# Kernel tuning notes

Hardware: AMD Instinct MI355X
Metric: run time of the kernel (lower is better)

The kernel has to match this reference:

```python
import jax, jax.numpy as jnp
import numpy as np
from jax import lax

B, P, ENC = 64, 196, 2048
E, H, A, V = 512, 512, 512, 10000
L = 21  # caption length -> T = 20 decode steps


def setup_inputs() -> dict:
    key = jax.random.key(0)
    ks = jax.random.split(key, 20)
    s = 0.02
    inp = {
        "features": jax.random.normal(ks[0], (B, P, ENC), jnp.float32),
        "captions": jax.random.randint(ks[1], (B, L), 0, V),
        # attention
        "W_enc_att": jax.random.normal(ks[2], (ENC, A), jnp.float32) * s,
        "b_enc_att": jnp.zeros((A,), jnp.float32),
        "W_dec_att": jax.random.normal(ks[3], (H, A), jnp.float32) * s,
        "b_dec_att": jnp.zeros((A,), jnp.float32),
        "W_full": jax.random.normal(ks[4], (A, 1), jnp.float32) * s,
        "b_full": jnp.zeros((1,), jnp.float32),
        # embedding (uniform(-0.1, 0.1) as in init_weights)
        "emb": jax.random.uniform(ks[5], (V, E), jnp.float32, -0.1, 0.1),
        # LSTMCell: input = embed + encoder_dim, gate order i,f,g,o
        "W_ih": jax.random.normal(ks[6], (E + ENC, 4 * H), jnp.float32) * s,
        "W_hh": jax.random.normal(ks[7], (H, 4 * H), jnp.float32) * s,
        "b_ih": jnp.zeros((4 * H,), jnp.float32),
        "b_hh": jnp.zeros((4 * H,), jnp.float32),
        # init state projections
        "W_init_h": jax.random.normal(ks[8], (ENC, H), jnp.float32) * s,
        "b_init_h": jnp.zeros((H,), jnp.float32),
        "W_init_c": jax.random.normal(ks[9], (ENC, H), jnp.float32) * s,
        "b_init_c": jnp.zeros((H,), jnp.float32),
        # gating
        "W_fbeta": jax.random.normal(ks[10], (H, ENC), jnp.float32) * s,
        "b_fbeta": jnp.zeros((ENC,), jnp.float32),
        # output fc (uniform(-0.1,0.1), bias 0)
        "W_fc": jax.random.uniform(ks[11], (H, V), jnp.float32, -0.1, 0.1),
        "b_fc": jnp.zeros((V,), jnp.float32),
    }
    return inp


def reference(features, captions, W_enc_att, b_enc_att, W_dec_att, b_dec_att,
              W_full, b_full, emb, W_ih, W_hh, b_ih, b_hh,
              W_init_h, b_init_h, W_init_c, b_init_c,
              W_fbeta, b_fbeta, W_fc, b_fc):
    # init hidden state from mean-pooled encoder features
    mean_enc = features.mean(axis=1)                       # [B, ENC]
    h0 = mean_enc @ W_init_h + b_init_h                    # [B, H]
    c0 = mean_enc @ W_init_c + b_init_c

    # encoder-side attention projection is time-invariant: precompute
    att1 = features @ W_enc_att + b_enc_att                # [B, P, A]

    T = captions.shape[1] - 1                              # decode_lengths = L-1 (equal lengths)
    embs = emb[captions[:, :T]]                            # [B, T, E]
    embs_t = jnp.swapaxes(embs, 0, 1)                      # [T, B, E]

    def step(carry, e_t):
        h, c = carry
        att2 = h @ W_dec_att + b_dec_att                   # [B, A]
        scores = (jax.nn.relu(att1 + att2[:, None, :]) @ W_full)[..., 0] + b_full  # [B, P]
        alpha = jax.nn.softmax(scores, axis=1)
        awe = jnp.einsum('bp,bpe->be', alpha, features)    # [B, ENC]
        gate = jax.nn.sigmoid(h @ W_fbeta + b_fbeta)
        awe = gate * awe
        x = jnp.concatenate([e_t, awe], axis=1)            # [B, E+ENC]
        gates = x @ W_ih + h @ W_hh + b_ih + b_hh          # [B, 4H]
        i, f, g, o = jnp.split(gates, 4, axis=1)
        c_new = jax.nn.sigmoid(f) * c + jax.nn.sigmoid(i) * jnp.tanh(g)
        h_new = jax.nn.sigmoid(o) * jnp.tanh(c_new)
        preds = h_new @ W_fc + b_fc                        # dropout in eval mode = identity
        return (h_new, c_new), preds

    _, preds = lax.scan(step, (h0, c0), embs_t)            # [T, B, V]
    return jnp.swapaxes(preds, 0, 1)                       # [B, T, V]
```

## Files before the change

kernel.cpp:

```cpp
#include <hip/hip_runtime.h>
#include <hip/hip_bf16.h>


#define TB 256

typedef __bf16 bf16x8 __attribute__((ext_vector_type(8)));
typedef float f32x4 __attribute__((ext_vector_type(4)));
typedef unsigned short u16x8 __attribute__((ext_vector_type(8)));
typedef unsigned short u16x4 __attribute__((ext_vector_type(4)));
typedef unsigned short ushort_t;

__device__ __forceinline__ ushort_t f2bf(float x) {
    unsigned u = __builtin_bit_cast(unsigned, x);
    u += 0x7fffu + ((u >> 16) & 1u);
    return (ushort_t)(u >> 16);
}
__device__ __forceinline__ float bf2f(ushort_t b) {
    return __builtin_bit_cast(float, (unsigned)b << 16);
}
__device__ __forceinline__ void store_pack(
    ushort_t* __restrict__ Ph, ushort_t* __restrict__ Pl,
    int KC, int m, int k, float v)
{
    const size_t flat = ((((size_t)(m >> 4) * KC + (k >> 5)) * 64)
                         + ((k & 31) >> 3) * 16 + (m & 15)) * 8 + (k & 7);
    const ushort_t h = f2bf(v);
    Ph[flat] = h;
    Pl[flat] = f2bf(v - bf2f(h));
}

struct PackJobs {
    const float* W[7];
    ushort_t* Bh[7];
    ushort_t* Bl[7];
    int Nsrc[7], ntCount[7], KC[7], ntBase[7];
    int cum[8];
};

__global__ __launch_bounds__(TB) void pack_all(PackJobs J)
{
    const int blk = blockIdx.x;
    int j = 0;
    #pragma unroll
    for (int i = 1; i < 7; ++i) if (blk >= J.cum[i]) j = i;
    const int g = (blk - J.cum[j]) * TB + threadIdx.x;
    const int KC = J.KC[j];
    const int lane = g & 63;
    const int kc = (g >> 6) % KC;
    const int nt = g / (64 * KC);
    if (nt >= J.ntCount[j]) return;
    const int Nsrc = J.Nsrc[j];
    const float* W = J.W[j];
    const int n = nt * 16 + (lane & 15);
    const int kb = kc * 32 + (lane >> 4) * 8;
    u16x8 hv, lv;
    #pragma unroll
    for (int e = 0; e < 8; ++e) {
        const float x = (n < Nsrc) ? W[(size_t)(kb + e) * Nsrc + n] : 0.f;
        const ushort_t h = f2bf(x);
        hv[e] = h;
        lv[e] = f2bf(x - bf2f(h));
    }
    const size_t flat = (((size_t)(J.ntBase[j] + nt) * KC + kc) * 64 + lane) * 8;
    *(u16x8*)&J.Bh[j][flat] = hv;
    *(u16x8*)&J.Bl[j][flat] = lv;
}

__global__ __launch_bounds__(TB) void feat2bf(
    const float* __restrict__ f, ushort_t* __restrict__ fbf)
{
    const size_t i8 = ((size_t)blockIdx.x * TB + threadIdx.x) * 8;
    const float4 a = *(const float4*)&f[i8];
    const float4 b = *(const float4*)&f[i8 + 4];
    u16x8 v;
    v[0] = f2bf(a.x); v[1] = f2bf(a.y); v[2] = f2bf(a.z); v[3] = f2bf(a.w);
    v[4] = f2bf(b.x); v[5] = f2bf(b.y); v[6] = f2bf(b.z); v[7] = f2bf(b.w);
    *(u16x8*)&fbf[i8] = v;
}

template<int MT, int NT, int WR, int WC>
__device__ __forceinline__ void mfma_tile(
    const ushort_t* lds, int wr, int wc, int lane,
    f32x4 acc[MT / WR][NT / WC])
{
    constexpr int MFR = MT / WR, NFR = NT / WC;
    bf16x8 ah[MFR], al[MFR];
    #pragma unroll
    for (int i = 0; i < MFR; ++i) {
        ah[i] = __builtin_bit_cast(bf16x8, *(const u16x8*)&lds[(wr * MFR + i) * 512 + lane * 8]);
        al[i] = __builtin_bit_cast(bf16x8, *(const u16x8*)&lds[(MT + wr * MFR + i) * 512 + lane * 8]);
    }
    #pragma unroll
    for (int j = 0; j < NFR; ++j) {
        const bf16x8 bh = __builtin_bit_cast(bf16x8, *(const u16x8*)&lds[(2 * MT + wc * NFR + j) * 512 + lane * 8]);
        const bf16x8 bl = __builtin_bit_cast(bf16x8, *(const u16x8*)&lds[(2 * MT + NT + wc * NFR + j) * 512 + lane * 8]);
        #pragma unroll
        for (int i = 0; i < MFR; ++i) {
            acc[i][j] = __builtin_amdgcn_mfma_f32_16x16x32_bf16(ah[i], bh, acc[i][j], 0, 0, 0);
            acc[i][j] = __builtin_amdgcn_mfma_f32_16x16x32_bf16(ah[i], bl, acc[i][j], 0, 0, 0);
            acc[i][j] = __builtin_amdgcn_mfma_f32_16x16x32_bf16(al[i], bh, acc[i][j], 0, 0, 0);
        }
    }
}

template<int MT, int NT, int WR, int WC>
__global__ __launch_bounds__(TB) void gemm_mfma(
    const ushort_t* __restrict__ Ah, const ushort_t* __restrict__ Al,
    const ushort_t* __restrict__ Bh, const ushort_t* __restrict__ Bl,
    int KC, int kcPer,
    const float* __restrict__ bias,
    float* __restrict__ C, int ldc, int Ncols, size_t cPartStride)
{
    constexpr int MFR = MT / WR, NFR = NT / WC, CH = 2 * (MT + NT);
    __shared__ __align__(16) ushort_t lds[CH * 512];
    const int tid = threadIdx.x, wid = tid >> 6, lane = tid & 63;
    const int wr = wid / WC, wc = wid % WC;

    const int tot = gridDim.x * gridDim.y;
    const int lin = blockIdx.x + gridDim.x * blockIdx.y;
    const int q = tot >> 3, r = tot & 7;
    const int xcd = lin & 7, jj = lin >> 3;
    const int base = (xcd < r) ? xcd * (q + 1) : r * (q + 1) + (xcd - r) * q;
    const int lin2 = base + jj;
    const int nb = lin2 / gridDim.y;
    const int mb = lin2 % gridDim.y;

    const int kc0 = blockIdx.z * kcPer;

    f32x4 acc[MFR][NFR];
    #pragma unroll
    for (int i = 0; i < MFR; ++i)
        #pragma unroll
        for (int j = 0; j < NFR; ++j)
            acc[i][j] = f32x4{0.f, 0.f, 0.f, 0.f};

    for (int kc = kc0; kc < kc0 + kcPer; ++kc) {
        __syncthreads();
        #pragma unroll
        for (int cc = 0; cc < CH / 4; ++cc) {
            const int c = cc * 4 + wid;
            const ushort_t* src;
            if (c < MT)                src = Ah + ((size_t)(mb * MT + c) * KC + kc) * 512;
            else if (c < 2 * MT)       src = Al + ((size_t)(mb * MT + c - MT) * KC + kc) * 512;
            else if (c < 2 * MT + NT)  src = Bh + ((size_t)(nb * NT + c - 2 * MT) * KC + kc) * 512;
            else                       src = Bl + ((size_t)(nb * NT + c - 2 * MT - NT) * KC + kc) * 512;
            *(u16x8*)&lds[c * 512 + lane * 8] = *(const u16x8*)(src + lane * 8);
        }
        __syncthreads();
        mfma_tile<MT, NT, WR, WC>(lds, wr, wc, lane, acc);
    }

    C += (size_t)blockIdx.z * cPartStride;
    #pragma unroll
    for (int i = 0; i < MFR; ++i)
        #pragma unroll
        for (int j = 0; j < NFR; ++j) {
            const int col = nb * NT * 16 + (wc * NFR + j) * 16 + (lane & 15);
            if (col < Ncols) {
                const float bv = bias ? bias[col] : 0.f;
                const int rbase = mb * MT * 16 + (wr * MFR + i) * 16 + ((lane >> 4) << 2);
                #pragma unroll
                for (int r2 = 0; r2 < 4; ++r2)
                    C[(size_t)(rbase + r2) * ldc + col] = acc[i][j][r2] + bv;
            }
        }
}

__global__ __launch_bounds__(TB) void gemm_att1(
    const ushort_t* __restrict__ fbf,
    const ushort_t* __restrict__ Bh, const ushort_t* __restrict__ Bl,
    const float* __restrict__ bias, ushort_t* __restrict__ att1bf)
{
    __shared__ __align__(16) ushort_t lds[2 * 16 * 512];
    const int tid = threadIdx.x, wid = tid >> 6, lane = tid & 63;
    const int wr = wid >> 1, wc = wid & 1;

    const int lin = blockIdx.x + (blockIdx.y << 3);
    const int lin2 = (lin & 7) * 98 + (lin >> 3);
    const int nb = lin2 & 7, mb = lin2 >> 3;

    f32x4 acc[4][2];
    #pragma unroll
    for (int i = 0; i < 4; ++i)
        #pragma unroll
        for (int j = 0; j < 2; ++j)
            acc[i][j] = f32x4{0.f, 0.f, 0.f, 0.f};

    const int akg = tid & 3;
    const size_t abase = (size_t)(mb * 128) * 2048;

    u16x8 rA[4], rB[4];

    auto issueTo = [&](int kc, u16x8* r) {
        #pragma unroll
        for (int cc = 0; cc < 2; ++cc) {
            const int c = cc * 4 + wid;
            const ushort_t* src = (c < 4)
                ? Bh + ((size_t)(nb * 4 + c) * 64 + kc) * 512
                : Bl + ((size_t)(nb * 4 + (c - 4)) * 64 + kc) * 512;
            r[cc] = *(const u16x8*)(src + lane * 8);
        }
        #pragma unroll
        for (int p = 0; p < 2; ++p) {
            const int row = (p * 256 + tid) >> 2;
            r[2 + p] = *(const u16x8*)&fbf[abase + (size_t)row * 2048 + (size_t)kc * 32 + akg * 8];
        }
    };
    auto commitFrom = [&](const u16x8* r, ushort_t* buf) {
        #pragma unroll
        for (int cc = 0; cc < 2; ++cc) {
            const int c = cc * 4 + wid;
            *(u16x8*)&buf[(8 + c) * 512 + lane * 8] = r[cc];
        }
        #pragma unroll
        for (int p = 0; p < 2; ++p) {
            const int row = (p * 256 + tid) >> 2;
            *(u16x8*)&buf[(row >> 4) * 512 + (akg * 16 + (row & 15)) * 8] = r[2 + p];
        }
    };
    auto compute = [&](const ushort_t* buf) {
        bf16x8 ah[4];
        #pragma unroll
        for (int i = 0; i < 4; ++i)
            ah[i] = __builtin_bit_cast(bf16x8, *(const u16x8*)&buf[(wr * 4 + i) * 512 + lane * 8]);
        #pragma unroll
        for (int j = 0; j < 2; ++j) {
            const bf16x8 bh = __builtin_bit_cast(bf16x8, *(const u16x8*)&buf[(8 + wc * 2 + j) * 512 + lane * 8]);
            const bf16x8 bl = __builtin_bit_cast(bf16x8, *(const u16x8*)&buf[(12 + wc * 2 + j) * 512 + lane * 8]);
            #pragma unroll
            for (int i = 0; i < 4; ++i) {
                acc[i][j] = __builtin_amdgcn_mfma_f32_16x16x32_bf16(ah[i], bh, acc[i][j], 0, 0, 0);
                acc[i][j] = __builtin_amdgcn_mfma_f32_16x16x32_bf16(ah[i], bl, acc[i][j], 0, 0, 0);
            }
        }
    };

    issueTo(0, rA);
    commitFrom(rA, lds);
    issueTo(1, rB);
    __syncthreads();

    for (int kc = 0; kc < 64; kc += 2) {
        if (kc + 2 < 64) issueTo(kc + 2, rA);
        compute(lds);
        commitFrom(rB, lds + 16 * 512);
        __syncthreads();
        if (kc + 3 < 64) issueTo(kc + 3, rB);
        compute(lds + 16 * 512);
        if (kc + 2 < 64) commitFrom(rA, lds);
        __syncthreads();
    }

    #pragma unroll
    for (int i = 0; i < 4; ++i)
        #pragma unroll
        for (int j = 0; j < 2; ++j) {
            const int col = nb * 64 + (wc * 2 + j) * 16 + (lane & 15);
            const float bv = bias[col];
            const int rbase = mb * 128 + (wr * 4 + i) * 16 + ((lane >> 4) << 2);
            #pragma unroll
            for (int r = 0; r < 4; ++r)
                att1bf[(size_t)(rbase + r) * 512 + col] = f2bf(acc[i][j][r] + bv);
        }
}

__device__ __forceinline__ void gemm_body(
    float (*As)[68], float (*Ws)[68],
    const float* __restrict__ A, int lda,
    const float* __restrict__ W, int ldw,
    float* __restrict__ C, int ldc,
    int nTile, int N, int K)
{
    const int tid = threadIdx.x;
    const int tn = tid & 15;
    const int tm = tid >> 4;
    const int n0 = nTile * 64;

    float acc[4][4] = {{0.f}};

    for (int k0 = 0; k0 < K; k0 += 32) {
        {
            int r  = tid >> 3;
            int cc = (tid & 7) * 4;
            #pragma unroll
            for (int rr = 0; rr < 64; rr += 32) {
                const float4 a = *(const float4*)&A[(size_t)(rr + r) * lda + (k0 + cc)];
                As[cc + 0][rr + r] = a.x;
                As[cc + 1][rr + r] = a.y;
                As[cc + 2][rr + r] = a.z;
                As[cc + 3][rr + r] = a.w;
            }
        }
        {
            int r  = tid >> 4;
            int cc = (tid & 15) * 4;
            #pragma unroll
            for (int rr = 0; rr < 32; rr += 16) {
                const float4 w = *(const float4*)&W[(size_t)(k0 + rr + r) * ldw + (n0 + cc)];
                *(float4*)&Ws[rr + r][cc] = w;
            }
        }
        __syncthreads();
        #pragma unroll
        for (int kk = 0; kk < 32; ++kk) {
            const float4 a = *(const float4*)&As[kk][tm * 4];
            const float4 w = *(const float4*)&Ws[kk][tn * 4];
            const float av[4] = {a.x, a.y, a.z, a.w};
            const float wv[4] = {w.x, w.y, w.z, w.w};
            #pragma unroll
            for (int i = 0; i < 4; ++i)
                #pragma unroll
                for (int j = 0; j < 4; ++j)
                    acc[i][j] = fmaf(av[i], wv[j], acc[i][j]);
        }
        __syncthreads();
    }

    #pragma unroll
    for (int i = 0; i < 4; ++i) {
        const int m = tm * 4 + i;
        #pragma unroll
        for (int j = 0; j < 4; ++j)
            C[(size_t)m * ldc + (n0 + tn * 4 + j)] = acc[i][j];
    }
}

__global__ __launch_bounds__(TB) void gemm_hc(
    const float* __restrict__ mean,
    const float* __restrict__ Wh0, const float* __restrict__ Wc0,
    float* __restrict__ h0p, float* __restrict__ c0p)
{
    __shared__ float As[32][68];
    __shared__ float Ws[32][68];
    const int ks = blockIdx.y & 7;
    const int which = blockIdx.y >> 3;
    const float* W = which ? Wc0 : Wh0;
    float* Cp = which ? c0p : h0p;
    gemm_body(As, Ws,
              mean + (size_t)ks * 256, 2048,
              W + (size_t)ks * 256 * 512, 512,
              Cp + (size_t)ks * 64 * 512, 512,
              blockIdx.x, 512, 256);
}

__global__ __launch_bounds__(TB) void scores_k(
    const ushort_t* __restrict__ att1bf,
    const float* __restrict__ hga_part,
    const float* __restrict__ bd,
    const float* __restrict__ Wfull,
    float* __restrict__ scores)
{
    const int b = blockIdx.x;
    const int tid = threadIdx.x;
    const int wave = tid >> 6;
    const int lane = tid & 63;

    __shared__ float a2[512];
    __shared__ float wf[512];

    for (int i = tid; i < 512; i += TB) {
        float v = bd[i];
        #pragma unroll
        for (int s = 0; s < 4; ++s)
            v += hga_part[(size_t)s * 64 * 4608 + (size_t)b * 4608 + i];
        a2[i] = v;
        wf[i] = Wfull[i];
    }
    __syncthreads();

    const int k0 = lane * 8;
    float a2r[8], wfr[8];
    #pragma unroll
    for (int e = 0; e < 8; ++e) { a2r[e] = a2[k0 + e]; wfr[e] = wf[k0 + e]; }

    const int p0 = blockIdx.y * 28 + wave * 7;
    #pragma unroll
    for (int pp = 0; pp < 7; ++pp) {
        const int p = p0 + pp;
        const u16x8 v = *(const u16x8*)&att1bf[((size_t)b * 196 + p) * 512 + k0];
        float s = 0.f;
        #pragma unroll
        for (int e = 0; e < 8; ++e)
            s = fmaf(fmaxf(bf2f(v[e]) + a2r[e], 0.f), wfr[e], s);
        #pragma unroll
        for (int o = 32; o; o >>= 1) s += __shfl_xor(s, o);
        if (lane == 0) scores[b * 196 + p] = s;
    }
}

__global__ __launch_bounds__(512) void awe_gate(
    const float* __restrict__ scores,
    const ushort_t* __restrict__ fbf,
    const float* __restrict__ hga_part,
    const float* __restrict__ bf,
    ushort_t* __restrict__ gPh, ushort_t* __restrict__ gPl)
{
    const int b = blockIdx.y, chunk = blockIdx.x;
    const int tid = threadIdx.x;
    const int q = tid >> 6, lane = tid & 63;

    __shared__ float al[196];
    __shared__ float redm[8], reds[8];
    __shared__ float smq[8][512];

    const float sv = (tid < 196) ? scores[b * 196 + tid] : -1e30f;
    float m = sv;
    #pragma unroll
    for (int o = 32; o; o >>= 1) m = fmaxf(m, __shfl_xor(m, o));
    if (lane == 0) redm[q] = m;
    __syncthreads();
    m = redm[0];
    #pragma unroll
    for (int i = 1; i < 8; ++i) m = fmaxf(m, redm[i]);

    const float e = (tid < 196) ? expf(sv - m) : 0.f;
    float s = e;
    #pragma unroll
    for (int o = 32; o; o >>= 1) s += __shfl_xor(s, o);
    if (lane == 0) reds[q] = s;
    __syncthreads();
    s = reds[0];
    #pragma unroll
    for (int i = 1; i < 8; ++i) s += reds[i];

    if (tid < 196) al[tid] = e / s;
    __syncthreads();

    const int col0 = chunk * 512 + lane * 8;
    const ushort_t* f = fbf + (size_t)b * 196 * 2048 + col0;
    float acc[8] = {0.f, 0.f, 0.f, 0.f, 0.f, 0.f, 0.f, 0.f};
    const int p0 = q * 25;
    const int pn = (q == 7) ? 21 : 25;
    for (int pp = 0; pp < pn; ++pp) {
        const float w = al[p0 + pp];
        const u16x8 v = *(const u16x8*)&f[(size_t)(p0 + pp) * 2048];
        #pragma unroll
        for (int ee = 0; ee < 8; ++ee)
            acc[ee] = fmaf(w, bf2f(v[ee]), acc[ee]);
    }
    *(f32x4*)&smq[q][lane * 8]     = f32x4{acc[0], acc[1], acc[2], acc[3]};
    *(f32x4*)&smq[q][lane * 8 + 4] = f32x4{acc[4], acc[5], acc[6], acc[7]};
    __syncthreads();

    const int eg = chunk * 512 + tid;
    float a = smq[0][tid];
    #pragma unroll
    for (int i = 1; i < 8; ++i) a += smq[i][tid];
    float gp = bf[eg];
    #pragma unroll
    for (int ss = 0; ss < 4; ++ss)
        gp += hga_part[(size_t)ss * 64 * 4608 + (size_t)b * 4608 + 512 + eg];
    const float gate = 1.f / (1.f + expf(-gp));
    store_pack(gPh, gPl, 64, b, eg, gate * a);
}

__global__ __launch_bounds__(TB) void lstm_pw(
    const float* __restrict__ gates_part,
    const float* __restrict__ hga_part,
    const float* __restrict__ eW,
    const float* __restrict__ b_hh,
    int t,
    float* __restrict__ c,
    ushort_t* __restrict__ hPh, ushort_t* __restrict__ hPl,
    ushort_t* __restrict__ sPh, ushort_t* __restrict__ sPl)
{
    const int idx = blockIdx.x * TB + threadIdx.x;
    const int b = idx >> 9;
    const int j = idx & 511;

    float g[4];
    #pragma unroll
    for (int comp = 0; comp < 4; ++comp) {
        const int col = comp * 512 + j;
        float v = b_hh[col] + eW[((size_t)b * 20 + t) * 2048 + col];
        #pragma unroll
        for (int s = 0; s < 8; ++s)
            v += gates_part[(size_t)s * 64 * 2048 + (size_t)b * 2048 + col];
        #pragma unroll
        for (int s = 0; s < 4; ++s)
            v += hga_part[(size_t)s * 64 * 4608 + (size_t)b * 4608 + 2560 + col];
        g[comp] = v;
    }
    const float si = 1.f / (1.f + expf(-g[0]));
    const float sf = 1.f / (1.f + expf(-g[1]));
    const float gg = tanhf(g[2]);
    const float so = 1.f / (1.f + expf(-g[3]));
    const float cn = sf * c[idx] + si * gg;
    c[idx] = cn;
    const float hn = so * tanhf(cn);
    store_pack(hPh, hPl, 16, b, j, hn);
    store_pack(sPh, sPl, 16, b * 20 + t, j, hn);
}

__global__ __launch_bounds__(TB) void mean_feat_bf(
    const ushort_t* __restrict__ fbf, float* __restrict__ mean_enc)
{
    const int b = blockIdx.y;
    const int e = blockIdx.x * TB + threadIdx.x;
    const ushort_t* f = fbf + (size_t)b * 196 * 2048 + e;
    float s = 0.f;
    #pragma unroll 4
    for (int p = 0; p < 196; ++p) s += bf2f(f[(size_t)p * 2048]);
    mean_enc[b * 2048 + e] = s * (1.f / 196.f);
}

__global__ __launch_bounds__(TB) void gather_emb_pack(
    const int* __restrict__ captions,
    const float* __restrict__ emb,
    ushort_t* __restrict__ Ph, ushort_t* __restrict__ Pl)
{
    const int bt = blockIdx.x;
    const int b = bt / 20;
    const int t = bt % 20;
    const int tok = captions[b * 21 + t];
    for (int e = threadIdx.x; e < 512; e += TB)
        store_pack(Ph, Pl, 16, bt, e, emb[(size_t)tok * 512 + e]);
}

__global__ __launch_bounds__(TB) void reduce_hc(
    const float* __restrict__ h0p, const float* __restrict__ c0p,
    const float* __restrict__ bh0, const float* __restrict__ bc0,
    ushort_t* __restrict__ hPh, ushort_t* __restrict__ hPl,
    float* __restrict__ c)
{
    const int idx = blockIdx.x * TB + threadIdx.x;
    const int half = idx >> 15;
    const int i = idx & 32767;
    const int j = i & 511;
    const float* P = half ? c0p : h0p;
    float v = half ? bc0[j] : bh0[j];
    #pragma unroll
    for (int s = 0; s < 8; ++s) v += P[(size_t)s * 64 * 512 + i];
    if (half) c[i] = v;
    else      store_pack(hPh, hPl, 16, i >> 9, j, v);
}

extern "C" void kernel_launch(void* const* d_in, const int* in_sizes, int n_in,
                              void* d_out, int out_size, void* d_ws, size_t ws_size,
                              hipStream_t stream)
{
    const float* features  = (const float*)d_in[0];
    const int*   captions  = (const int*)  d_in[1];
    const float* W_enc_att = (const float*)d_in[2];
    const float* b_enc_att = (const float*)d_in[3];
    const float* W_dec_att = (const float*)d_in[4];
    const float* b_dec_att = (const float*)d_in[5];
    const float* W_full    = (const float*)d_in[6];
    const float* emb       = (const float*)d_in[8];
    const float* W_ih      = (const float*)d_in[9];
    const float* W_hh      = (const float*)d_in[10];
    const float* b_ih      = (const float*)d_in[11];
    const float* b_hh      = (const float*)d_in[12];
    const float* W_init_h  = (const float*)d_in[13];
    const float* b_init_h  = (const float*)d_in[14];
    const float* W_init_c  = (const float*)d_in[15];
    const float* b_init_c  = (const float*)d_in[16];
    const float* W_fbeta   = (const float*)d_in[17];
    const float* b_fbeta   = (const float*)d_in[18];
    const float* W_fc      = (const float*)d_in[19];
    const float* b_fc      = (const float*)d_in[20];
    float* out = (float*)d_out;
    (void)ws_size;

    float* ws = (float*)d_ws;
    size_t off = 0;
    auto alloc  = [&](size_t n) { float* p = ws + off; off += n; return p; };
    auto ualloc = [&](size_t n) { ushort_t* p = (ushort_t*)(ws + off); off += (n + 1) / 2; return p; };

    float* eW     = alloc((size_t)64 * 20 * 2048);
    float* mean   = alloc(64 * 2048);
    float* hga    = alloc((size_t)4 * 64 * 4608);
    float* gatesp = alloc((size_t)8 * 64 * 2048);
    float* c      = alloc(64 * 512);
    float* scores = alloc(64 * 196);

    ushort_t* fbf    = ualloc((size_t)12544 * 2048);
    ushort_t* att1bf = ualloc((size_t)12544 * 512);
    ushort_t* WencH = ualloc((size_t)32 * 64 * 512);
    ushort_t* WencL = ualloc((size_t)32 * 64 * 512);
    ushort_t* WtopH = ualloc((size_t)128 * 16 * 512);
    ushort_t* WtopL = ualloc((size_t)128 * 16 * 512);
    ushort_t* Wih2H = ualloc((size_t)128 * 64 * 512);
    ushort_t* Wih2L = ualloc((size_t)128 * 64 * 512);
    ushort_t* WdfhH = ualloc((size_t)288 * 16 * 512);
    ushort_t* WdfhL = ualloc((size_t)288 * 16 * 512);
    ushort_t* WfcH  = ualloc((size_t)632 * 16 * 512);
    ushort_t* WfcL  = ualloc((size_t)632 * 16 * 512);
    ushort_t* embsH = ualloc((size_t)80 * 16 * 512);
    ushort_t* embsL = ualloc((size_t)80 * 16 * 512);
    ushort_t* hPh   = ualloc((size_t)4 * 16 * 512);
    ushort_t* hPl   = ualloc((size_t)4 * 16 * 512);
    ushort_t* gPh   = ualloc((size_t)4 * 64 * 512);
    ushort_t* gPl   = ualloc((size_t)4 * 64 * 512);
    ushort_t* sPh   = ualloc((size_t)80 * 16 * 512);
    ushort_t* sPl   = ualloc((size_t)80 * 16 * 512);

    float* h0p = hga;
    float* c0p = gatesp;

    PackJobs J;
    J.W[0]=W_enc_att;               J.Bh[0]=WencH; J.Bl[0]=WencL; J.Nsrc[0]=512;   J.ntCount[0]=32;  J.KC[0]=64; J.ntBase[0]=0;
    J.W[1]=W_ih;                    J.Bh[1]=WtopH; J.Bl[1]=WtopL; J.Nsrc[1]=2048;  J.ntCount[1]=128; J.KC[1]=16; J.ntBase[1]=0;
    J.W[2]=W_ih + (size_t)512*2048; J.Bh[2]=Wih2H; J.Bl[2]=Wih2L; J.Nsrc[2]=2048;  J.ntCount[2]=128; J.KC[2]=64; J.ntBase[2]=0;
    J.W[3]=W_dec_att;               J.Bh[3]=WdfhH; J.Bl[3]=WdfhL; J.Nsrc[3]=512;   J.ntCount[3]=32;  J.KC[3]=16; J.ntBase[3]=0;
    J.W[4]=W_fbeta;                 J.Bh[4]=WdfhH; J.Bl[4]=WdfhL; J.Nsrc[4]=2048;  J.ntCount[4]=128; J.KC[4]=16; J.ntBase[4]=32;
    J.W[5]=W_hh;                    J.Bh[5]=WdfhH; J.Bl[5]=WdfhL; J.Nsrc[5]=2048;  J.ntCount[5]=128; J.KC[5]=16; J.ntBase[5]=160;
    J.W[6]=W_fc;                    J.Bh[6]=WfcH;  J.Bl[6]=WfcL;  J.Nsrc[6]=10000; J.ntCount[6]=632; J.KC[6]=16; J.ntBase[6]=0;
    {
        int cum = 0;
        const int blks[7] = {512, 512, 2048, 128, 512, 512, 2528};
        for (int i = 0; i < 7; ++i) { J.cum[i] = cum; cum += blks[i]; }
        J.cum[7] = cum;
        pack_all<<<cum, TB, 0, stream>>>(J);
    }

    feat2bf<<<12544, TB, 0, stream>>>(features, fbf);
    gather_emb_pack<<<1280, TB, 0, stream>>>(captions, emb, embsH, embsL);
    mean_feat_bf<<<dim3(8, 64), TB, 0, stream>>>(fbf, mean);
    gemm_hc<<<dim3(8, 16), TB, 0, stream>>>(mean, W_init_h, W_init_c, h0p, c0p);
    reduce_hc<<<256, TB, 0, stream>>>(h0p, c0p, b_init_h, b_init_c, hPh, hPl, c);
    gemm_att1<<<dim3(8, 98), TB, 0, stream>>>(fbf, WencH, WencL, b_enc_att, att1bf);
    gemm_mfma<8, 8, 2, 2><<<dim3(16, 10, 1), TB, 0, stream>>>(
        embsH, embsL, WtopH, WtopL, 16, 16, b_ih, eW, 2048, 2048, 0);

    for (int t = 0; t < 20; ++t) {
        gemm_mfma<4, 8, 2, 2><<<dim3(36, 1, 4), TB, 0, stream>>>(
            hPh, hPl, WdfhH, WdfhL, 16, 4, nullptr, hga, 4608, 4608, (size_t)64 * 4608);
        scores_k<<<dim3(64, 7), TB, 0, stream>>>(att1bf, hga, b_dec_att, W_full, scores);
        awe_gate<<<dim3(4, 64), 512, 0, stream>>>(scores, fbf, hga, b_fbeta, gPh, gPl);
        gemm_mfma<4, 8, 2, 2><<<dim3(16, 1, 8), TB, 0, stream>>>(
            gPh, gPl, Wih2H, Wih2L, 64, 8, nullptr, gatesp, 2048, 2048, (size_t)64 * 2048);
        lstm_pw<<<128, TB, 0, stream>>>(gatesp, hga, eW, b_hh, t, c, hPh, hPl, sPh, sPl);
    }

    gemm_mfma<8, 8, 2, 2><<<dim3(79, 10, 1), TB, 0, stream>>>(
        sPh, sPl, WfcH, WfcL, 16, 16, b_fc, out, 10000, 10000, 0);
}
```

Measured before the change: 1.036 ms.

## Fuse attention scores, softmax, and gated context into one per-batch kernel

Replaces the separate scores and attention-weighted-encoding kernels with a single kernel per batch row that computes scores into shared memory, applies softmax, accumulates the weighted feature sum over all 2048 columns in two halves, and applies the sigmoid gate. This removes one launch per decode step and the global round-trip for scores. The trade-off is the grid shrinking to 64 blocks, so far fewer CUs share the large feature and att1 reads.

```diff
diff --git a/kernel.cpp b/kernel.cpp
--- a/kernel.cpp
+++ b/kernel.cpp
@@ -343,39 +343,41 @@
               blockIdx.x, 512, 256);
 }
 
-__global__ __launch_bounds__(TB) void scores_k(
+__global__ __launch_bounds__(512) void attn_fused64(
     const ushort_t* __restrict__ att1bf,
-    const float* __restrict__ hga_part,
+    const float* __restrict__ hga,
     const float* __restrict__ bd,
     const float* __restrict__ Wfull,
-    float* __restrict__ scores)
+    const ushort_t* __restrict__ fbf,
+    const float* __restrict__ bfb,
+    ushort_t* __restrict__ gPh, ushort_t* __restrict__ gPl)
 {
     const int b = blockIdx.x;
-    const int tid = threadIdx.x;
-    const int wave = tid >> 6;
-    const int lane = tid & 63;
-
-    __shared__ float a2[512];
+    const int tid = threadIdx.x, w = tid >> 6, lane = tid & 63;
+
+    __shared__ float att2[512];
     __shared__ float wf[512];
-
-    for (int i = tid; i < 512; i += TB) {
-        float v = bd[i];
+    __shared__ float sc[200];
+    __shared__ float redm[8], reds[8];
+    __shared__ float smq[8][1024];
+
+    {
+        float v = bd[tid];
         #pragma unroll
         for (int s = 0; s < 4; ++s)
-            v += hga_part[(size_t)s * 64 * 4608 + (size_t)b * 4608 + i];
-        a2[i] = v;
-        wf[i] = Wfull[i];
+            v += hga[(size_t)s * 64 * 4608 + (size_t)b * 4608 + tid];
+        att2[tid] = v;
+        wf[tid] = Wfull[tid];
     }
     __syncthreads();
 
+    const int p0 = (w < 4) ? w * 25 : 100 + (w - 4) * 24;
+    const int pn = (w < 4) ? 25 : 24;
     const int k0 = lane * 8;
     float a2r[8], wfr[8];
     #pragma unroll
-    for (int e = 0; e < 8; ++e) { a2r[e] = a2[k0 + e]; wfr[e] = wf[k0 + e]; }
-
-    const int p0 = blockIdx.y * 28 + wave * 7;
-    #pragma unroll
-    for (int pp = 0; pp < 7; ++pp) {
+    for (int e = 0; e < 8; ++e) { a2r[e] = att2[k0 + e]; wfr[e] = wf[k0 + e]; }
+    for (int pp = 0; pp < pn; ++pp) {
         const int p = p0 + pp;
         const u16x8 v = *(const u16x8*)&att1bf[((size_t)b * 196 + p) * 512 + k0];
         float s = 0.f;
@@ -384,74 +386,69 @@
             s = fmaf(fmaxf(bf2f(v[e]) + a2r[e], 0.f), wfr[e], s);
         #pragma unroll
         for (int o = 32; o; o >>= 1) s += __shfl_xor(s, o);
-        if (lane == 0) scores[b * 196 + p] = s;
-    }
-}
-
-__global__ __launch_bounds__(512) void awe_gate(
-    const float* __restrict__ scores,
-    const ushort_t* __restrict__ fbf,
-    const float* __restrict__ hga_part,
-    const float* __restrict__ bf,
-    ushort_t* __restrict__ gPh, ushort_t* __restrict__ gPl)
-{
-    const int b = blockIdx.y, chunk = blockIdx.x;
-    const int tid = threadIdx.x;
-    const int q = tid >> 6, lane = tid & 63;
-
-    __shared__ float al[196];
-    __shared__ float redm[8], reds[8];
-    __shared__ float smq[8][512];
-
-    const float sv = (tid < 196) ? scores[b * 196 + tid] : -1e30f;
+        if (lane == 0) sc[p] = s;
+    }
+    __syncthreads();
+
+    const float sv = (tid < 196) ? sc[tid] : -1e30f;
     float m = sv;
     #pragma unroll
     for (int o = 32; o; o >>= 1) m = fmaxf(m, __shfl_xor(m, o));
-    if (lane == 0) redm[q] = m;
+    if (lane == 0) redm[w] = m;
     __syncthreads();
     m = redm[0];
     #pragma unroll
     for (int i = 1; i < 8; ++i) m = fmaxf(m, redm[i]);
-
     const float e = (tid < 196) ? expf(sv - m) : 0.f;
     float s = e;
     #pragma unroll
     for (int o = 32; o; o >>= 1) s += __shfl_xor(s, o);
-    if (lane == 0) reds[q] = s;
+    if (lane == 0) reds[w] = s;
     __syncthreads();
     s = reds[0];
     #pragma unroll
     for (int i = 1; i < 8; ++i) s += reds[i];
-
-    if (tid < 196) al[tid] = e / s;
+    if (tid < 196) sc[tid] = e / s;
     __syncthreads();
 
-    const int col0 = chunk * 512 + lane * 8;
-    const ushort_t* f = fbf + (size_t)b * 196 * 2048 + col0;
-    float acc[8] = {0.f, 0.f, 0.f, 0.f, 0.f, 0.f, 0.f, 0.f};
-    const int p0 = q * 25;
-    const int pn = (q == 7) ? 21 : 25;
-    for (int pp = 0; pp < pn; ++pp) {
-        const float w = al[p0 + pp];
-        const u16x8 v = *(const u16x8*)&f[(size_t)(p0 + pp) * 2048];
-        #pragma unroll
-        for (int ee = 0; ee < 8; ++ee)
-            acc[ee] = fmaf(w, bf2f(v[ee]), acc[ee]);
-    }
-    *(f32x4*)&smq[q][lane * 8]     = f32x4{acc[0], acc[1], acc[2], acc[3]};
-    *(f32x4*)&smq[q][lane * 8 + 4] = f32x4{acc[4], acc[5], acc[6], acc[7]};
-    __syncthreads();
-
-    const int eg = chunk * 512 + tid;
-    float a = smq[0][tid];
-    #pragma unroll
-    for (int i = 1; i < 8; ++i) a += smq[i][tid];
-    float gp = bf[eg];
-    #pragma unroll
-    for (int ss = 0; ss < 4; ++ss)
-        gp += hga_part[(size_t)ss * 64 * 4608 + (size_t)b * 4608 + 512 + eg];
-    const float gate = 1.f / (1.f + expf(-gp));
-    store_pack(gPh, gPl, 64, b, eg, gate * a);
+    #pragma unroll
+    for (int half = 0; half < 2; ++half) {
+        const int colbase = half * 1024;
+        const ushort_t* f = fbf + (size_t)b * 196 * 2048 + colbase + lane * 8;
+        float acc[16];
+        #pragma unroll
+        for (int x = 0; x < 16; ++x) acc[x] = 0.f;
+        for (int pp = 0; pp < pn; ++pp) {
+            const float wgt = sc[p0 + pp];
+            const u16x8 v0 = *(const u16x8*)&f[(size_t)(p0 + pp) * 2048];
+            const u16x8 v1 = *(const u16x8*)&f[(size_t)(p0 + pp) * 2048 + 512];
+            #pragma unroll
+            for (int ee = 0; ee < 8; ++ee) {
+                acc[ee]     = fmaf(wgt, bf2f(v0[ee]), acc[ee]);
+                acc[8 + ee] = fmaf(wgt, bf2f(v1[ee]), acc[8 + ee]);
+            }
+        }
+        *(f32x4*)&smq[w][lane * 8]           = f32x4{acc[0], acc[1], acc[2], acc[3]};
+        *(f32x4*)&smq[w][lane * 8 + 4]       = f32x4{acc[4], acc[5], acc[6], acc[7]};
+        *(f32x4*)&smq[w][512 + lane * 8]     = f32x4{acc[8], acc[9], acc[10], acc[11]};
+        *(f32x4*)&smq[w][512 + lane * 8 + 4] = f32x4{acc[12], acc[13], acc[14], acc[15]};
+        __syncthreads();
+
+        #pragma unroll
+        for (int x = tid; x < 1024; x += 512) {
+            float a = smq[0][x];
+            #pragma unroll
+            for (int i = 1; i < 8; ++i) a += smq[i][x];
+            const int cg = colbase + x;
+            float gp = bfb[cg];
+            #pragma unroll
+            for (int ss = 0; ss < 4; ++ss)
+                gp += hga[(size_t)ss * 64 * 4608 + (size_t)b * 4608 + 512 + cg];
+            const float gate = 1.f / (1.f + expf(-gp));
+            store_pack(gPh, gPl, 64, b, cg, gate * a);
+        }
+        __syncthreads();
+    }
 }
 
 __global__ __launch_bounds__(TB) void lstm_pw(
@@ -572,7 +569,6 @@
     float* hga    = alloc((size_t)4 * 64 * 4608);
     float* gatesp = alloc((size_t)8 * 64 * 2048);
     float* c      = alloc(64 * 512);
-    float* scores = alloc(64 * 196);
 
     ushort_t* fbf    = ualloc((size_t)12544 * 2048);
     ushort_t* att1bf = ualloc((size_t)12544 * 512);
@@ -626,8 +622,8 @@
     for (int t = 0; t < 20; ++t) {
         gemm_mfma<4, 8, 2, 2><<<dim3(36, 1, 4), TB, 0, stream>>>(
             hPh, hPl, WdfhH, WdfhL, 16, 4, nullptr, hga, 4608, 4608, (size_t)64 * 4608);
-        scores_k<<<dim3(64, 7), TB, 0, stream>>>(att1bf, hga, b_dec_att, W_full, scores);
-        awe_gate<<<dim3(4, 64), 512, 0, stream>>>(scores, fbf, hga, b_fbeta, gPh, gPl);
+        attn_fused64<<<64, 512, 0, stream>>>(
+            att1bf, hga, b_dec_att, W_full, fbf, b_fbeta, gPh, gPl);
         gemm_mfma<4, 8, 2, 2><<<dim3(16, 1, 8), TB, 0, stream>>>(
             gPh, gPl, Wih2H, Wih2L, 64, 8, nullptr, gatesp, 2048, 2048, (size_t)64 * 2048);
         lstm_pw<<<128, TB, 0, stream>>>(gatesp, hga, eW, b_hh, t, c, hPh, hPl, sPh, sPl);
```

After: 1.257 ms. 21.3% more time.
